# Kernel tuning notes

Hardware: AMD Instinct MI355X
Metric: run time of the kernel (lower is better)

The kernel has to match this reference:

```python
import jax, jax.numpy as jnp
import numpy as np

B, N, C = 8, 1024, 768      # batch, tokens, dim
H, HD = 8, 96               # num_heads (= top-k experts per token), head_dim
E, T = 24, 9                # num_experts, task_num
SCALE = HD ** -0.5
W_SWITCH, W_Z = 0.1, 0.001  # switchloss, zloss weights from __init__ defaults


def setup_inputs() -> dict:
    key = jax.random.key(0)
    ks = jax.random.split(key, 5)
    g = lambda k, sh, sc: jax.random.normal(k, sh, dtype=jnp.float32) * sc
    return {
        "x": g(ks[0], (B, N, C), 1.0),
        "W_gate": g(ks[1], (T, C, E), C ** -0.5),   # per-task gating weights
        "W_in": g(ks[2], (E, C, HD), C ** -0.5),    # expert q projections (TaskMoE.map)
        "W_out": g(ks[3], (E, HD, C), HD ** -0.5),  # expert output projections (TaskMoE.reduce)
        "W_kv": g(ks[4], (C, 2 * HD), C ** -0.5),   # shared kv_proj (MQA-style)
        "task_bh": 3,
    }


def reference(x, W_gate, W_in, W_out, W_kv, task_bh):
    # ---- task-conditioned top-k gating (eval path: no noise, no sampling) ----
    logits = jnp.einsum('bnc,ce->bne', x, W_gate[task_bh])          # [B,N,E]
    probs = jax.nn.softmax(logits, axis=-1)
    top_g, top_i = jax.lax.top_k(probs, H)                          # [B,N,H]
    top_g = top_g / (jnp.sum(top_g, axis=-1, keepdims=True) + 1e-6)
    # ---- TaskMoE.map: per-head q = selected expert projection of x ----
    q_all = jnp.einsum('bnc,ecd->bned', x, W_in)                    # [B,N,E,HD]
    q = jnp.take_along_axis(q_all, top_i[..., None], axis=2)        # [B,N,H,HD]
    # ---- shared K/V (single head) ----
    kv = x @ W_kv                                                   # [B,N,2*HD]
    k, v = kv[..., :HD], kv[..., HD:]
    # ---- MQA attention ----
    attn = jnp.einsum('bihd,bjd->bhij', q, k) * SCALE               # [B,H,N,N]
    attn = jax.nn.softmax(attn, axis=-1)
    o = jnp.einsum('bhij,bjd->bihd', attn, v)                       # [B,N,H,HD]
    # ---- TaskMoE.reduce: gate-weighted combine through output experts ----
    onehot = jax.nn.one_hot(top_i, E, dtype=o.dtype)                # [B,N,H,E]
    z = jnp.einsum('bnhd,bnhe,bnh->bned', o, onehot, top_g)         # [B,N,E,HD]
    out = jnp.einsum('bned,edc->bnc', z, W_out)                     # [B,N,C]
    # ---- auxiliary routing losses (switch load-balance + z-loss) ----
    importance = probs.mean(axis=(0, 1))                            # [E]
    load = onehot.sum(axis=2).mean(axis=(0, 1)) / H                 # [E]
    switchloss = E * jnp.sum(importance * load)
    zloss = jnp.mean(jax.nn.logsumexp(logits, axis=-1) ** 2)
    aux_loss = W_SWITCH * switchloss + W_Z * zloss
    return out, aux_loss
```

## Files before the change

### kernel.cpp

```cpp
#include <hip/hip_runtime.h>
#include <hip/hip_bf16.h>
#include <math.h>

#define BB 8
#define NN 1024
#define CC 768
#define HH 8
#define HD 96
#define EE 24
#define NT (BB*NN)
#define NSLOT (NT*HH)
#define EC (EE*HD)
#define CAPQ 8192
#define ASCALE 0.10206207261596575f
#define AL2 0.14724446f
#define DEFER_THR 11.5415603f

typedef unsigned short u16;
typedef unsigned char u8;
typedef unsigned int u32;
typedef unsigned long long u64;
typedef __attribute__((ext_vector_type(8))) short s16x8;
typedef __attribute__((ext_vector_type(4))) float f32x4;
typedef __attribute__((ext_vector_type(16))) float f32x16;

__device__ __forceinline__ u16 f2b(float f) {
  unsigned u = __builtin_bit_cast(unsigned, f);
  unsigned r = u + 0x7fffu + ((u >> 16) & 1u);
  return (u16)(r >> 16);
}

__device__ __forceinline__ float fexp2(float x) {
  float r; asm("v_exp_f32 %0, %1" : "=v"(r) : "v"(x)); return r;
}

__device__ __forceinline__ u32 cvtpk(float a, float b) {
  u32 d; asm("v_cvt_pk_bf16_f32 %0, %1, %2" : "=v"(d) : "v"(a), "v"(b)); return d;
}

__device__ __forceinline__ void gload16(const u16* g, u16* lds) {
  __builtin_amdgcn_global_load_lds(
      (const __attribute__((address_space(1))) void*)g,
      (__attribute__((address_space(3))) void*)lds, 16, 0, 0);
}

__device__ __forceinline__ int xcd_remap(int bid, int nwg) {
  int q = nwg >> 3, r = nwg & 7;
  int xcd = bid & 7, idx = bid >> 3;
  return (xcd < r ? xcd * (q + 1) : r * (q + 1) + (xcd - r) * q) + idx;
}

#define WS_CNT   0
#define WS_IMP   96
#define WS_ZSUM  192
#define WS_G     256
#define WS_EID   (WS_G + NSLOT*4)
#define WS_KVK   (WS_EID + NSLOT)
#define WS_VT    (WS_KVK + NT*128*2)
#define WS_WIN   (WS_VT + (size_t)96*NT*2)
#define WS_WOUT  (WS_WIN + (size_t)EC*CC*2)
#define WS_WKV   (WS_WOUT + (size_t)CC*EC*2)
#define WS_QA    (WS_WKV + 192*CC*2)
#define WS_Z     (WS_QA + (size_t)NT*EC*2)
#define WS_XB    WS_Z
#define WS_BUCKET (WS_Z + (size_t)16*1024*1024)

__global__ __launch_bounds__(512) void gate_kernel(
    const float* __restrict__ x, const float* __restrict__ Wg_all,
    const int* __restrict__ task_p, float* __restrict__ ws_f,
    int* __restrict__ ws_i, u8* __restrict__ eids, u16* __restrict__ xb,
    int* __restrict__ bucket)
{
  __shared__ float xs[32][65];
  __shared__ float wgs[64][24];
  __shared__ float scr[4][32][6];
  __shared__ float lgt[32][26];
  __shared__ float zlo[32];
  __shared__ int hist[EE];
  __shared__ int gbase[EE];

  int t = threadIdx.x;
  int w = t >> 6, l = t & 63;
  int eg = w & 3, e0 = eg * 6;
  int r = l & 31;
  int q = ((w >> 2) << 1) | (l >> 5);
  int tok0 = blockIdx.x * 32;
  const float* Wg = Wg_all + (size_t)task_p[0] * CC * EE;

  if (t < EE) hist[t] = 0;

  float acc[6];
  #pragma unroll
  for (int c = 0; c < 6; c++) acc[c] = 0.f;

  for (int kb = 0; kb < CC; kb += 64) {
    __syncthreads();
    {
      int rr = t >> 4, cc = (t & 15) << 2;
      float4 v = *(const float4*)&x[(size_t)(tok0 + rr) * CC + kb + cc];
      *(float4*)&xs[rr][cc] = v;
      u64 pk = (u64)f2b(v.x) | ((u64)f2b(v.y) << 16) |
               ((u64)f2b(v.z) << 32) | ((u64)f2b(v.w) << 48);
      *(u64*)&xb[(size_t)(tok0 + rr) * CC + kb + cc] = pk;
    }
    #pragma unroll
    for (int i = 0; i < 2; i++) {
      int idx = i * 512 + t;
      if (idx < 768) {
        int kk = idx / 12, c2 = idx % 12;
        *(float2*)&wgs[kk][c2 * 2] = *(const float2*)&Wg[(size_t)(kb + kk) * EE + c2 * 2];
      }
    }
    __syncthreads();
    int k0 = q * 16;
    #pragma unroll
    for (int k = 0; k < 16; k++) {
      float xv = xs[r][k0 + k];
      float2 w01 = *(const float2*)&wgs[k0 + k][e0];
      float2 w23 = *(const float2*)&wgs[k0 + k][e0 + 2];
      float2 w45 = *(const float2*)&wgs[k0 + k][e0 + 4];
      acc[0] += xv * w01.x; acc[1] += xv * w01.y;
      acc[2] += xv * w23.x; acc[3] += xv * w23.y;
      acc[4] += xv * w45.x; acc[5] += xv * w45.y;
    }
  }
  #pragma unroll
  for (int c = 0; c < 6; c++) acc[c] += __shfl_xor(acc[c], 32);
  if (w >= 4 && l < 32) {
    #pragma unroll
    for (int c = 0; c < 6; c++) scr[eg][r][c] = acc[c];
  }
  __syncthreads();
  if (w < 4 && l < 32) {
    #pragma unroll
    for (int c = 0; c < 6; c++) lgt[r][e0 + c] = acc[c] + scr[eg][r][c];
  }
  __syncthreads();

  int my_e[8], loc[8];
  if (t < 32) {
    int token = tok0 + t;
    float lg[EE];
    #pragma unroll
    for (int e = 0; e < EE; e++) lg[e] = lgt[t][e];
    float mx = lg[0];
    #pragma unroll
    for (int e = 1; e < EE; e++) mx = fmaxf(mx, lg[e]);
    float se = 0.f; float probs[EE];
    #pragma unroll
    for (int e = 0; e < EE; e++) { probs[e] = __expf(lg[e] - mx); se += probs[e]; }
    float inv = 1.f / se;
    #pragma unroll
    for (int e = 0; e < EE; e++) probs[e] *= inv;
    float lse = mx + __logf(se);
    zlo[t] = lse * lse;

    unsigned taken = 0u;
    float gsum = 0.f;
    float my_g[8];
    #pragma unroll
    for (int h = 0; h < HH; h++) {
      float best = -1.f; int bi = 0;
      #pragma unroll
      for (int e = 0; e < EE; e++) {
        bool ok = !((taken >> e) & 1u) && (probs[e] > best);
        best = ok ? probs[e] : best;
        bi   = ok ? e : bi;
      }
      taken |= 1u << bi;
      gsum += best;
      my_g[h] = best; my_e[h] = bi;
    }
    float ginv = 1.f / (gsum + 1e-6f);
    float4 g0, g1;
    g0.x = my_g[0] * ginv; g0.y = my_g[1] * ginv; g0.z = my_g[2] * ginv; g0.w = my_g[3] * ginv;
    g1.x = my_g[4] * ginv; g1.y = my_g[5] * ginv; g1.z = my_g[6] * ginv; g1.w = my_g[7] * ginv;
    float* gbuf = ws_f + WS_G / 4;
    *(float4*)&gbuf[(size_t)token * HH]     = g0;
    *(float4*)&gbuf[(size_t)token * HH + 4] = g1;
    u64 pk = 0;
    #pragma unroll
    for (int h = 0; h < HH; h++) pk |= (u64)(u8)my_e[h] << (8 * h);
    *(u64*)&eids[(size_t)token * HH] = pk;
    #pragma unroll
    for (int h = 0; h < HH; h++) loc[h] = atomicAdd(&hist[my_e[h]], 1);
    #pragma unroll
    for (int e = 0; e < EE; e++) lgt[t][e] = probs[e];
  }
  __syncthreads();
  if (t < EE) {
    float s = 0.f;
    #pragma unroll 8
    for (int rr = 0; rr < 32; rr++) s += lgt[rr][t];
    atomicAdd(ws_f + WS_IMP / 4 + t, s);
    gbase[t] = atomicAdd(&ws_i[t], hist[t]);
  } else if (t == 32) {
    float s = 0.f;
    #pragma unroll 8
    for (int rr = 0; rr < 32; rr++) s += zlo[rr];
    atomicAdd(ws_f + WS_ZSUM / 4, s);
  }
  __syncthreads();
  if (t < 32) {
    int token = tok0 + t;
    #pragma unroll
    for (int h = 0; h < HH; h++)
      bucket[my_e[h] * CAPQ + gbase[my_e[h]] + loc[h]] = token;
  }
}

__global__ __launch_bounds__(256) void transpose_kernel(
    const float* __restrict__ src, u16* __restrict__ dst,
    int R, int C, int sB, int dR, int dB)
{
  __shared__ float tile[32][33];
  int e = blockIdx.z;
  const float* s = src + (size_t)e * sB;
  int t = threadIdx.x;
  int tr = t >> 5, tc = t & 31;
  #pragma unroll
  for (int i = 0; i < 4; i++) {
    int r = blockIdx.x * 32 + tr + i * 8;
    int c = blockIdx.y * 32 + tc;
    tile[tr + i * 8][tc] = s[(size_t)r * C + c];
  }
  __syncthreads();
  #pragma unroll
  for (int i = 0; i < 4; i++) {
    int sc = blockIdx.y * 32 + tr + i * 8;
    int sr = blockIdx.x * 32 + tc;
    dst[(size_t)e * dB + (size_t)sc * dR + sr] = f2b(tile[tc][tr + i * 8]);
  }
}

template<int BM, int BN, bool OUT_F32>
__global__ __launch_bounds__(256) void gemm_kernel(
    const u16* __restrict__ A, const u16* __restrict__ Bt,
    void* __restrict__ Cp, int M, int N, int K)
{
  constexpr int WM = BM / 2, WN = BN / 2;
  constexpr int FM = WM / 16, FN = WN / 16;
  __shared__ u16 As[BM][64];
  __shared__ u16 Bs[BN][64];
  int t = threadIdx.x;
  int w = t >> 6, l = t & 63;
  int lr = l & 15, lg = l >> 4;
  int wr = w >> 1, wc = w & 1;
  int nwg = gridDim.x * gridDim.y;
  int logical = xcd_remap(blockIdx.y * gridDim.x + blockIdx.x, nwg);
  int col0 = (logical % gridDim.x) * BN, row0 = (logical / gridDim.x) * BM;

  f32x4 acc[FM][FN];
  #pragma unroll
  for (int i = 0; i < FM; i++)
    #pragma unroll
    for (int j = 0; j < FN; j++) acc[i][j] = (f32x4)(0.f);

  int sr = t >> 3;
  int sc = t & 7;
  for (int kb = 0; kb < K; kb += 64) {
    __syncthreads();
    #pragma unroll
    for (int i = 0; i < BM / 32; i++) {
      int rr = i * 32 + sr;
      int ch = sc ^ (rr & 7);
      gload16(A + (size_t)(row0 + rr) * K + kb + ch * 8, &As[rr][sc * 8]);
    }
    #pragma unroll
    for (int i = 0; i < BN / 32; i++) {
      int rr = i * 32 + sr;
      int ch = sc ^ (rr & 7);
      gload16(Bt + (size_t)(col0 + rr) * K + kb + ch * 8, &Bs[rr][sc * 8]);
    }
    __syncthreads();
    #pragma unroll
    for (int ks = 0; ks < 2; ks++) {
      s16x8 af[FM], bf[FN];
      #pragma unroll
      for (int i = 0; i < FM; i++)
        af[i] = *(const s16x8*)&As[wr * WM + i * 16 + lr][8 * ((ks * 4 + lg) ^ (lr & 7))];
      #pragma unroll
      for (int j = 0; j < FN; j++)
        bf[j] = *(const s16x8*)&Bs[wc * WN + j * 16 + lr][8 * ((ks * 4 + lg) ^ (lr & 7))];
      #pragma unroll
      for (int i = 0; i < FM; i++)
        #pragma unroll
        for (int j = 0; j < FN; j++)
          acc[i][j] = __builtin_amdgcn_mfma_f32_16x16x32_bf16(af[i], bf[j], acc[i][j], 0, 0, 0);
    }
  }
  #pragma unroll
  for (int i = 0; i < FM; i++)
    #pragma unroll
    for (int j = 0; j < FN; j++)
      #pragma unroll
      for (int reg = 0; reg < 4; reg++) {
        int rr = row0 + wr * WM + i * 16 + lg * 4 + reg;
        int cc = col0 + wc * WN + j * 16 + lr;
        if (OUT_F32) ((float*)Cp)[(size_t)rr * N + cc] = acc[i][j][reg];
        else ((u16*)Cp)[(size_t)rr * N + cc] = f2b(acc[i][j][reg]);
      }
}

__global__ __launch_bounds__(256) void qproj_kernel(
    const u16* __restrict__ xb, const u16* __restrict__ winT,
    const int* __restrict__ ws_i, const int* __restrict__ bucket,
    u16* __restrict__ qall)
{
  int e = blockIdx.y;
  int t0 = blockIdx.x * 128;
  int cnt = ws_i[e];
  if (t0 >= cnt) return;
  __shared__ u16 As[128][64];
  __shared__ u16 Bs[96][64];
  __shared__ int tok_s[128];
  int t = threadIdx.x;
  if (t < 128) tok_s[t] = bucket[e * CAPQ + min(t0 + t, cnt - 1)];
  __syncthreads();
  int w = t >> 6, l = t & 63;
  int lr = l & 15, lg = l >> 4;
  int wr = w >> 1, wc = w & 1;
  const u16* Bt = winT + (size_t)e * HD * CC;

  f32x4 acc[4][3];
  #pragma unroll
  for (int i = 0; i < 4; i++)
    #pragma unroll
    for (int j = 0; j < 3; j++) acc[i][j] = (f32x4)(0.f);

  int sr = t >> 3, sc = t & 7;
  int atok[4];
  #pragma unroll
  for (int i = 0; i < 4; i++) atok[i] = tok_s[i * 32 + sr];

  for (int kb = 0; kb < CC; kb += 64) {
    __syncthreads();
    #pragma unroll
    for (int i = 0; i < 4; i++) {
      int rr = i * 32 + sr;
      int ch = sc ^ (rr & 7);
      gload16(xb + (size_t)atok[i] * CC + kb + ch * 8, &As[rr][sc * 8]);
    }
    #pragma unroll
    for (int i = 0; i < 3; i++) {
      int rr = i * 32 + sr;
      int ch = sc ^ (rr & 7);
      gload16(Bt + (size_t)rr * CC + kb + ch * 8, &Bs[rr][sc * 8]);
    }
    __syncthreads();
    #pragma unroll
    for (int ks = 0; ks < 2; ks++) {
      s16x8 af[4], bf[3];
      #pragma unroll
      for (int i = 0; i < 4; i++)
        af[i] = *(const s16x8*)&As[wr * 64 + i * 16 + lr][8 * ((ks * 4 + lg) ^ (lr & 7))];
      #pragma unroll
      for (int j = 0; j < 3; j++)
        bf[j] = *(const s16x8*)&Bs[wc * 48 + j * 16 + lr][8 * ((ks * 4 + lg) ^ (lr & 7))];
      #pragma unroll
      for (int i = 0; i < 4; i++)
        #pragma unroll
        for (int j = 0; j < 3; j++)
          acc[i][j] = __builtin_amdgcn_mfma_f32_16x16x32_bf16(af[i], bf[j], acc[i][j], 0, 0, 0);
    }
  }
  #pragma unroll
  for (int i = 0; i < 4; i++)
    #pragma unroll
    for (int reg = 0; reg < 4; reg++) {
      int rr = wr * 64 + i * 16 + lg * 4 + reg;
      if (t0 + rr < cnt) {
        int tok = tok_s[rr];
        u16* qp = qall + (size_t)tok * EC + e * HD + wc * 48;
        #pragma unroll
        for (int j = 0; j < 3; j++)
          qp[j * 16 + lr] = f2b(acc[i][j][reg]);
      }
    }
}

__global__ __launch_bounds__(256) void kvproj_kernel(
    const u16* __restrict__ xb, const u16* __restrict__ wkvT,
    u16* __restrict__ kvbk, u16* __restrict__ vtb)
{
  __shared__ u16 As[128][64];
  __shared__ u16 Bs[64][64];
  int t = threadIdx.x;
  int w = t >> 6, l = t & 63;
  int lr = l & 15, lg = l >> 4;
  int wr = w >> 1, wc = w & 1;
  int nwg = gridDim.x * gridDim.y;
  int logical = xcd_remap(blockIdx.y * gridDim.x + blockIdx.x, nwg);
  int col0 = (logical % gridDim.x) * 64, row0 = (logical / gridDim.x) * 128;

  f32x4 acc[4][2];
  #pragma unroll
  for (int i = 0; i < 4; i++)
    #pragma unroll
    for (int j = 0; j < 2; j++) acc[i][j] = (f32x4)(0.f);

  int sr = t >> 3, sc = t & 7;
  for (int kb = 0; kb < CC; kb += 64) {
    __syncthreads();
    #pragma unroll
    for (int i = 0; i < 4; i++) {
      int rr = i * 32 + sr;
      int ch = sc ^ (rr & 7);
      gload16(xb + (size_t)(row0 + rr) * CC + kb + ch * 8, &As[rr][sc * 8]);
    }
    #pragma unroll
    for (int i = 0; i < 2; i++) {
      int rr = i * 32 + sr;
      int ch = sc ^ (rr & 7);
      gload16(wkvT + (size_t)(col0 + rr) * CC + kb + ch * 8, &Bs[rr][sc * 8]);
    }
    __syncthreads();
    #pragma unroll
    for (int ks = 0; ks < 2; ks++) {
      s16x8 af[4], bf[2];
      #pragma unroll
      for (int i = 0; i < 4; i++)
        af[i] = *(const s16x8*)&As[wr * 64 + i * 16 + lr][8 * ((ks * 4 + lg) ^ (lr & 7))];
      #pragma unroll
      for (int j = 0; j < 2; j++)
        bf[j] = *(const s16x8*)&Bs[wc * 32 + j * 16 + lr][8 * ((ks * 4 + lg) ^ (lr & 7))];
      #pragma unroll
      for (int i = 0; i < 4; i++)
        #pragma unroll
        for (int j = 0; j < 2; j++)
          acc[i][j] = __builtin_amdgcn_mfma_f32_16x16x32_bf16(af[i], bf[j], acc[i][j], 0, 0, 0);
    }
  }
  #pragma unroll
  for (int i = 0; i < 4; i++)
    #pragma unroll
    for (int j = 0; j < 2; j++) {
      int cb = col0 + wc * 32 + j * 16 + lr;
      int rb = row0 + wr * 64 + i * 16 + lg * 4;
      if (cb < 96) {
        int ch = cb >> 3, ci = cb & 7;
        #pragma unroll
        for (int reg = 0; reg < 4; reg++) {
          int tok = rb + reg;
          kvbk[(size_t)tok * 128 + 8 * (ch ^ (tok & 7)) + ci] = f2b(acc[i][j][reg]);
        }
      } else {
        int d = cb - 96;
        u64 pk = (u64)f2b(acc[i][j][0]) | ((u64)f2b(acc[i][j][1]) << 16) |
                 ((u64)f2b(acc[i][j][2]) << 32) | ((u64)f2b(acc[i][j][3]) << 48);
        int blkbase = rb & ~63;
        int ch = (rb & 63) >> 3;
        *(u64*)&vtb[(size_t)d * NT + blkbase + 8 * (ch ^ (d & 7)) + (rb & 7)] = pk;
      }
    }
}

__global__ __launch_bounds__(256, 2) void attn_kernel(
    const u16* __restrict__ qall, const u16* __restrict__ kvbk,
    const u16* __restrict__ vtb, const u8* __restrict__ eids,
    const float* __restrict__ gbuf, u16* __restrict__ z)
{
  __shared__ u16 Ks[2][64][128];
  __shared__ u16 Vt[2][96][64];
  int b = blockIdx.y;
  int tok0 = blockIdx.x * 32;
  int t = threadIdx.x;
  int w = t >> 6, l = t & 63;
  int h = blockIdx.z * 4 + w;
  int lo = l & 31, hi = l >> 5;

  s16x8 qf[6];
  {
    int tok = b * NN + tok0 + lo;
    int e = eids[tok * HH + h];
    const u16* qp = qall + (size_t)tok * EC + e * HD + hi * 8;
    #pragma unroll
    for (int ks = 0; ks < 6; ks++)
      qf[ks] = *(const s16x8*)(qp + ks * 16);
  }

  const u16* kvwin = kvbk + (size_t)(b * NN) * 128;
  const u16* vwin  = vtb + (size_t)(b * NN);

  f32x16 o0 = (f32x16)(0.f), o1 = (f32x16)(0.f), o2 = (f32x16)(0.f);
  float m = -1e30f, lsum = 0.f;

  #pragma unroll
  for (int k2 = 0; k2 < 4; k2++) {
    int c = t + k2 * 256;
    gload16(kvwin + c * 8, &Ks[0][0][0] + c * 8);
  }
  #pragma unroll
  for (int k2 = 0; k2 < 3; k2++) {
    int c = t + k2 * 256;
    gload16(vwin + (size_t)(c >> 3) * NT + (c & 7) * 8, &Vt[0][0][0] + c * 8);
  }

  for (int jt = 0; jt < 16; jt++) {
    __syncthreads();
    if (jt < 15) {
      int j0 = (jt + 1) * 64;
      int nb = (jt + 1) & 1;
      const u16* kb_ = kvwin + (size_t)j0 * 128;
      #pragma unroll
      for (int k2 = 0; k2 < 4; k2++) {
        int c = t + k2 * 256;
        gload16(kb_ + c * 8, &Ks[nb][0][0] + c * 8);
      }
      const u16* vb_ = vwin + j0;
      #pragma unroll
      for (int k2 = 0; k2 < 3; k2++) {
        int c = t + k2 * 256;
        gload16(vb_ + (size_t)(c >> 3) * NT + (c & 7) * 8, &Vt[nb][0][0] + c * 8);
      }
    }
    int buf = jt & 1;

    f32x16 s0 = (f32x16)(0.f), s1 = (f32x16)(0.f);
    #pragma unroll
    for (int ks = 0; ks < 6; ks++) {
      int pos = 8 * ((2 * ks + hi) ^ (lo & 7));
      s16x8 a0 = *(const s16x8*)&Ks[buf][lo][pos];
      s16x8 a1 = *(const s16x8*)&Ks[buf][32 + lo][pos];
      s0 = __builtin_amdgcn_mfma_f32_32x32x16_bf16(a0, qf[ks], s0, 0, 0, 0);
      s1 = __builtin_amdgcn_mfma_f32_32x32x16_bf16(a1, qf[ks], s1, 0, 0, 0);
    }

    float pm = fmaxf(s0[0], s0[1]);
    #pragma unroll
    for (int rg = 2; rg < 16; rg += 2) pm = fmaxf(pm, fmaxf(s0[rg], s0[rg + 1]));
    #pragma unroll
    for (int rg = 0; rg < 16; rg += 2) pm = fmaxf(pm, fmaxf(s1[rg], s1[rg + 1]));
    pm = fmaxf(pm, __shfl_xor(pm, 32));
    pm *= AL2;

    if (!__all(pm - m <= DEFER_THR)) {
      float mn = fmaxf(m, pm);
      float al = fexp2(m - mn);
      m = mn; lsum *= al;
      #pragma unroll
      for (int rg = 0; rg < 16; rg++) {
        int qrow = (rg & 3) + 8 * (rg >> 2) + 4 * hi;
        float alr = __shfl(al, qrow);
        o0[rg] *= alr; o1[rg] *= alr; o2[rg] *= alr;
      }
    }

    float ts = 0.f;
    u32 wpk[2][4][2];
    #pragma unroll
    for (int kb2 = 0; kb2 < 2; kb2++)
      #pragma unroll
      for (int rr = 0; rr < 4; rr++)
        #pragma unroll
        for (int pp = 0; pp < 2; pp++) {
          float sA = kb2 ? s1[rr * 4 + 2 * pp]     : s0[rr * 4 + 2 * pp];
          float sB = kb2 ? s1[rr * 4 + 2 * pp + 1] : s0[rr * 4 + 2 * pp + 1];
          float eA = fexp2(fmaf(sA, AL2, -m));
          float eB = fexp2(fmaf(sB, AL2, -m));
          ts += eA + eB;
          wpk[kb2][rr][pp] = cvtpk(eA, eB);
        }
    lsum += ts;

    s16x8 pa[4];
    #pragma unroll
    for (int ks = 0; ks < 4; ks++) {
      int kb2 = ks >> 1;
      int rlo = (ks & 1) * 2, rhi = rlo + 1;
      u32 own_lo0 = wpk[kb2][rlo][0], own_lo1 = wpk[kb2][rlo][1];
      u32 own_hi0 = wpk[kb2][rhi][0], own_hi1 = wpk[kb2][rhi][1];
      u32 send0 = hi ? own_lo0 : own_hi0;
      u32 send1 = hi ? own_lo1 : own_hi1;
      u32 recv0 = (u32)__shfl_xor((int)send0, 32);
      u32 recv1 = (u32)__shfl_xor((int)send1, 32);
      union { s16x8 v; u32 u[4]; } pu;
      pu.u[0] = hi ? recv0 : own_lo0;
      pu.u[1] = hi ? recv1 : own_lo1;
      pu.u[2] = hi ? own_hi0 : recv0;
      pu.u[3] = hi ? own_hi1 : recv1;
      pa[ks] = pu.v;
    }

    #pragma unroll
    for (int ks = 0; ks < 4; ks++) {
      int pos = 8 * ((2 * ks + hi) ^ (lo & 7));
      s16x8 v0 = *(const s16x8*)&Vt[buf][lo][pos];
      s16x8 v1 = *(const s16x8*)&Vt[buf][32 + lo][pos];
      s16x8 v2 = *(const s16x8*)&Vt[buf][64 + lo][pos];
      o0 = __builtin_amdgcn_mfma_f32_32x32x16_bf16(pa[ks], v0, o0, 0, 0, 0);
      o1 = __builtin_amdgcn_mfma_f32_32x32x16_bf16(pa[ks], v1, o1, 0, 0, 0);
      o2 = __builtin_amdgcn_mfma_f32_32x32x16_bf16(pa[ks], v2, o2, 0, 0, 0);
    }
  }

  float lt = lsum + __shfl_xor(lsum, 32);
  #pragma unroll
  for (int rg = 0; rg < 16; rg++) {
    int qrow = (rg & 3) + 8 * (rg >> 2) + 4 * hi;
    float lv = __shfl(lt, qrow);
    int tok = b * NN + tok0 + qrow;
    int slot = tok * HH + h;
    float scl = gbuf[slot] / lv;
    int e = eids[slot];
    u16* zp = z + (size_t)tok * EC + e * HD + lo;
    zp[0]  = f2b(o0[rg] * scl);
    zp[32] = f2b(o1[rg] * scl);
    zp[64] = f2b(o2[rg] * scl);
  }
}

__global__ void aux_kernel(const float* __restrict__ ws_f,
                           const int* __restrict__ ws_i, float* __restrict__ out)
{
  if (threadIdx.x == 0 && blockIdx.x == 0) {
    float sw = 0.f;
    for (int e = 0; e < EE; e++) {
      float imp = ws_f[WS_IMP / 4 + e] / (float)NT;
      float load = (float)ws_i[e] / (float)(NT * HH);
      sw += imp * load;
    }
    float zl = ws_f[WS_ZSUM / 4] / (float)NT;
    out[(size_t)NT * CC] = 0.1f * ((float)EE * sw) + 0.001f * zl;
  }
}

extern "C" void kernel_launch(void* const* d_in, const int* in_sizes, int n_in,
                              void* d_out, int out_size, void* d_ws, size_t ws_size,
                              hipStream_t stream)
{
  const float* x    = (const float*)d_in[0];
  const float* Wg   = (const float*)d_in[1];
  const float* Win  = (const float*)d_in[2];
  const float* Wout = (const float*)d_in[3];
  const float* Wkv  = (const float*)d_in[4];
  const int*   task = (const int*)d_in[5];
  float* out = (float*)d_out;
  float* ws_f = (float*)d_ws;
  int*   ws_i = (int*)d_ws;
  u8*  eids = (u8*)((char*)d_ws + WS_EID);
  u16* kvbk = (u16*)((char*)d_ws + WS_KVK);
  u16* vtb  = (u16*)((char*)d_ws + WS_VT);
  u16* winT = (u16*)((char*)d_ws + WS_WIN);
  u16* woutT= (u16*)((char*)d_ws + WS_WOUT);
  u16* wkvT = (u16*)((char*)d_ws + WS_WKV);
  u16* qall = (u16*)((char*)d_ws + WS_QA);
  u16* z    = (u16*)((char*)d_ws + WS_Z);
  u16* xb   = (u16*)((char*)d_ws + WS_XB);
  int* bucket = (int*)((char*)d_ws + WS_BUCKET);

  hipMemsetAsync(d_ws, 0, 256, stream);

  transpose_kernel<<<dim3(CC/32, HD/32, EE), 256, 0, stream>>>(Win, winT, CC, HD, CC*HD, CC, HD*CC);
  transpose_kernel<<<dim3(HD/32, CC/32, EE), 256, 0, stream>>>(Wout, woutT, HD, CC, HD*CC, EC, HD);
  transpose_kernel<<<dim3(CC/32, 192/32, 1), 256, 0, stream>>>(Wkv, wkvT, CC, 192, 0, CC, 0);

  gate_kernel<<<NT / 32, 512, 0, stream>>>(x, Wg, task, ws_f, ws_i, eids, xb, bucket);

  kvproj_kernel<<<dim3(3, NT/128), 256, 0, stream>>>(xb, wkvT, kvbk, vtb);
  qproj_kernel<<<dim3(NT/128, EE), 256, 0, stream>>>(xb, winT, ws_i, bucket, qall);

  hipMemsetAsync(z, 0, (size_t)NT * EC * 2, stream);

  attn_kernel<<<dim3(NN/32, BB, 2), 256, 0, stream>>>(qall, kvbk, vtb, eids, ws_f + WS_G/4, z);

  gemm_kernel<128, 64, true><<<dim3(CC/64, NT/128), 256, 0, stream>>>(
      z, woutT, out, NT, CC, EC);

  aux_kernel<<<1, 64, 0, stream>>>(ws_f, ws_i, out);
}
```

Measured before the change: 178.8 us.

## Restructure gate kernel into 16-token blocks with register-tiled 4x6 outer products

```diff
diff --git a/kernel.cpp b/kernel.cpp
--- a/kernel.cpp
+++ b/kernel.cpp
@@ -65,33 +65,36 @@
 #define WS_XB    WS_Z
 #define WS_BUCKET (WS_Z + (size_t)16*1024*1024)
 
-__global__ __launch_bounds__(512) void gate_kernel(
+__global__ __launch_bounds__(256) void gate_kernel(
     const float* __restrict__ x, const float* __restrict__ Wg_all,
     const int* __restrict__ task_p, float* __restrict__ ws_f,
     int* __restrict__ ws_i, u8* __restrict__ eids, u16* __restrict__ xb,
     int* __restrict__ bucket)
 {
-  __shared__ float xs[32][65];
-  __shared__ float wgs[64][24];
-  __shared__ float scr[4][32][6];
-  __shared__ float lgt[32][26];
-  __shared__ float zlo[32];
+  __shared__ float xs[16][68];
+  __shared__ float wgt[24][68];
+  __shared__ float scr[4][16][24];
+  __shared__ float lgt[16][26];
+  __shared__ float zlo[16];
   __shared__ int hist[EE];
   __shared__ int gbase[EE];
 
   int t = threadIdx.x;
   int w = t >> 6, l = t & 63;
-  int eg = w & 3, e0 = eg * 6;
-  int r = l & 31;
-  int q = ((w >> 2) << 1) | (l >> 5);
-  int tok0 = blockIdx.x * 32;
+  int pos = l & 15;
+  int tg = pos >> 2, eg = pos & 3;
+  int kq_low = (l >> 4) & 3;
+  int cq = 16 * w + 4 * kq_low;
+  int tok0 = blockIdx.x * 16;
   const float* Wg = Wg_all + (size_t)task_p[0] * CC * EE;
 
   if (t < EE) hist[t] = 0;
 
-  float acc[6];
-  #pragma unroll
-  for (int c = 0; c < 6; c++) acc[c] = 0.f;
+  float acc[4][6];
+  #pragma unroll
+  for (int i = 0; i < 4; i++)
+    #pragma unroll
+    for (int j = 0; j < 6; j++) acc[i][j] = 0.f;
 
   for (int kb = 0; kb < CC; kb += 64) {
     __syncthreads();
@@ -104,41 +107,59 @@
       *(u64*)&xb[(size_t)(tok0 + rr) * CC + kb + cc] = pk;
     }
     #pragma unroll
-    for (int i = 0; i < 2; i++) {
-      int idx = i * 512 + t;
-      if (idx < 768) {
-        int kk = idx / 12, c2 = idx % 12;
-        *(float2*)&wgs[kk][c2 * 2] = *(const float2*)&Wg[(size_t)(kb + kk) * EE + c2 * 2];
-      }
-    }
-    __syncthreads();
-    int k0 = q * 16;
-    #pragma unroll
-    for (int k = 0; k < 16; k++) {
-      float xv = xs[r][k0 + k];
-      float2 w01 = *(const float2*)&wgs[k0 + k][e0];
-      float2 w23 = *(const float2*)&wgs[k0 + k][e0 + 2];
-      float2 w45 = *(const float2*)&wgs[k0 + k][e0 + 4];
-      acc[0] += xv * w01.x; acc[1] += xv * w01.y;
-      acc[2] += xv * w23.x; acc[3] += xv * w23.y;
-      acc[4] += xv * w45.x; acc[5] += xv * w45.y;
-    }
-  }
-  #pragma unroll
-  for (int c = 0; c < 6; c++) acc[c] += __shfl_xor(acc[c], 32);
-  if (w >= 4 && l < 32) {
-    #pragma unroll
-    for (int c = 0; c < 6; c++) scr[eg][r][c] = acc[c];
+    for (int i = 0; i < 6; i++) {
+      int f = t + i * 256;
+      int kk = f / 24, e = f - kk * 24;
+      wgt[e][kk] = Wg[(size_t)(kb + kk) * EE + e];
+    }
+    __syncthreads();
+    float4 x4[4];
+    #pragma unroll
+    for (int i = 0; i < 4; i++) x4[i] = *(const float4*)&xs[tg * 4 + i][cq];
+    #pragma unroll
+    for (int j = 0; j < 6; j++) {
+      float4 w4 = *(const float4*)&wgt[eg * 6 + j][cq];
+      #pragma unroll
+      for (int i = 0; i < 4; i++) {
+        float a = acc[i][j];
+        a = fmaf(x4[i].x, w4.x, a);
+        a = fmaf(x4[i].y, w4.y, a);
+        a = fmaf(x4[i].z, w4.z, a);
+        a = fmaf(x4[i].w, w4.w, a);
+        acc[i][j] = a;
+      }
+    }
+  }
+  #pragma unroll
+  for (int i = 0; i < 4; i++)
+    #pragma unroll
+    for (int j = 0; j < 6; j++) {
+      float v = acc[i][j];
+      v += __shfl_xor(v, 16);
+      v += __shfl_xor(v, 32);
+      acc[i][j] = v;
+    }
+  if (l < 16) {
+    #pragma unroll
+    for (int i = 0; i < 4; i++)
+      #pragma unroll
+      for (int j = 0; j < 6; j++) scr[w][pos][i * 6 + j] = acc[i][j];
   }
   __syncthreads();
-  if (w < 4 && l < 32) {
-    #pragma unroll
-    for (int c = 0; c < 6; c++) lgt[r][e0 + c] = acc[c] + scr[eg][r][c];
+  if (w == 0 && l < 16) {
+    #pragma unroll
+    for (int i = 0; i < 4; i++)
+      #pragma unroll
+      for (int j = 0; j < 6; j++) {
+        float s = scr[0][pos][i * 6 + j] + scr[1][pos][i * 6 + j] +
+                  scr[2][pos][i * 6 + j] + scr[3][pos][i * 6 + j];
+        lgt[tg * 4 + i][eg * 6 + j] = s;
+      }
   }
   __syncthreads();
 
   int my_e[8], loc[8];
-  if (t < 32) {
+  if (t < 16) {
     int token = tok0 + t;
     float lg[EE];
     #pragma unroll
@@ -191,17 +212,17 @@
   if (t < EE) {
     float s = 0.f;
     #pragma unroll 8
-    for (int rr = 0; rr < 32; rr++) s += lgt[rr][t];
+    for (int rr = 0; rr < 16; rr++) s += lgt[rr][t];
     atomicAdd(ws_f + WS_IMP / 4 + t, s);
     gbase[t] = atomicAdd(&ws_i[t], hist[t]);
   } else if (t == 32) {
     float s = 0.f;
     #pragma unroll 8
-    for (int rr = 0; rr < 32; rr++) s += zlo[rr];
+    for (int rr = 0; rr < 16; rr++) s += zlo[rr];
     atomicAdd(ws_f + WS_ZSUM / 4, s);
   }
   __syncthreads();
-  if (t < 32) {
+  if (t < 16) {
     int token = tok0 + t;
     #pragma unroll
     for (int h = 0; h < HH; h++)
@@ -655,7 +676,7 @@
   transpose_kernel<<<dim3(HD/32, CC/32, EE), 256, 0, stream>>>(Wout, woutT, HD, CC, HD*CC, EC, HD);
   transpose_kernel<<<dim3(CC/32, 192/32, 1), 256, 0, stream>>>(Wkv, wkvT, CC, 192, 0, CC, 0);
 
-  gate_kernel<<<NT / 32, 512, 0, stream>>>(x, Wg, task, ws_f, ws_i, eids, xb, bucket);
+  gate_kernel<<<NT / 16, 256, 0, stream>>>(x, Wg, task, ws_f, ws_i, eids, xb, bucket);
 
   kvproj_kernel<<<dim3(3, NT/128), 256, 0, stream>>>(xb, wkvT, kvbk, vtb);
   qproj_kernel<<<dim3(NT/128, EE), 256, 0, stream>>>(xb, winT, ws_i, bucket, qall);
```

After: 191.8 us. +7.3%, slower.
